# Optimization experiments

Hardware: AMD Instinct MI355X
Metric: run time of the kernel (lower is better)

Reference implementation:

```python
import jax, jax.numpy as jnp
import numpy as np

EMB_DIM = 1024
NUM_HEAD = 16
HEAD_DIM = EMB_DIM // NUM_HEAD
B, S = 2, 2048


def setup_inputs() -> dict:
    key = jax.random.key(0)
    ks = jax.random.split(key, 10)
    scale = 1.0 / np.sqrt(EMB_DIM)
    x = jax.random.normal(ks[0], (B, S, EMB_DIM), dtype=jnp.float32)
    # causal mask: 1 = keep, 0 = masked out (torch masked_fill(mask == 0, -inf))
    mask = jnp.tril(jnp.ones((S, S), dtype=jnp.int32))[None, None, :, :]
    def lin(kw, kb):
        W = jax.random.uniform(kw, (EMB_DIM, EMB_DIM), jnp.float32, -scale, scale)
        b = jax.random.uniform(kb, (EMB_DIM,), jnp.float32, -scale, scale)
        return W, b
    Wq, bq = lin(ks[1], ks[2])
    Wk, bk = lin(ks[3], ks[4])
    Wv, bv = lin(ks[5], ks[6])
    Wo, bo = lin(ks[7], ks[8])
    return {"x": x, "mask": mask, "Wq": Wq, "bq": bq, "Wk": Wk, "bk": bk,
            "Wv": Wv, "bv": bv, "Wo": Wo, "bo": bo}


def reference(x, mask, Wq, bq, Wk, bk, Wv, bv, Wo, bo):
    Bsz, Sq, _ = x.shape
    # projections; torch Linear: y = x @ W^T + b
    def proj(W, b):
        y = jnp.einsum('bse,fe->bsf', x, W) + b
        return y.reshape(Bsz, Sq, NUM_HEAD, HEAD_DIM).transpose(0, 2, 1, 3)  # [B,H,S,D]
    q = proj(Wq, bq)
    k = proj(Wk, bk)
    v = proj(Wv, bv)
    scaling = jnp.asarray(HEAD_DIM ** 0.5, x.dtype)
    scores = jnp.einsum('bhqd,bhkd->bhqk', q, k) / scaling  # [B,H,S,S]
    scores = jnp.where(mask == 0, -jnp.inf, scores)
    attn = jax.nn.softmax(scores, axis=-1)
    out = jnp.einsum('bhqk,bhkd->bhqd', attn, v)
    out = out.transpose(0, 2, 1, 3).reshape(Bsz, Sq, EMB_DIM)
    return jnp.einsum('bse,fe->bsf', out, Wo) + bo
```

## Files before the change

### kernel.cpp

```cpp
#include <hip/hip_runtime.h>

typedef unsigned short u16;
typedef __attribute__((ext_vector_type(8))) __bf16 bf16x8;
typedef __attribute__((ext_vector_type(8))) short  short8;
typedef __attribute__((ext_vector_type(4))) short  short4v;
typedef __attribute__((ext_vector_type(4))) float  floatx4;
typedef __attribute__((ext_vector_type(4))) int    intx4;

constexpr int Bc = 2, Sc = 2048, Ec = 1024, Hc = 16, Dc = 64;
constexpr int Mc = Bc * Sc;

#define QSCALE  0.18033688011112042f

__device__ __forceinline__ u16 f2b(float f) {
  union { float f; unsigned u; } c; c.f = f;
  unsigned u = c.u;
  return (u16)((u + 0x7fffu + ((u >> 16) & 1u)) >> 16);
}
__device__ __forceinline__ short8 ld8(const u16* p) { return *(const short8*)p; }

__device__ __forceinline__ int cvt_pk(float lo, float hi) {
  int r;
  asm("v_cvt_pk_bf16_f32 %0, %1, %2" : "=v"(r) : "v"(lo), "v"(hi));
  return r;
}

__device__ __forceinline__ floatx4 mfma16(short8 a, short8 b, floatx4 c) {
  return __builtin_amdgcn_mfma_f32_16x16x32_bf16(
      __builtin_bit_cast(bf16x8, a), __builtin_bit_cast(bf16x8, b), c, 0, 0, 0);
}

__device__ __forceinline__ void async16(const u16* g, u16* l) {
  __builtin_amdgcn_global_load_lds(
      (const __attribute__((address_space(1))) void*)g,
      (__attribute__((address_space(3))) void*)l, 16, 0, 0);
}

__global__ __launch_bounds__(256) void cvt_kernel(
    const float* __restrict__ x,  const float* __restrict__ Wq,
    const float* __restrict__ Wk, const float* __restrict__ Wv,
    const float* __restrict__ Wo, u16* __restrict__ dst) {
  const size_t i = ((size_t)blockIdx.x * 256 + threadIdx.x) * 4;
  const int seg = (int)(i >> 20);
  const float* src;
  size_t off;
  if (seg < 4)       { src = x;  off = i; }
  else if (seg == 4) { src = Wq; off = i - ((size_t)4 << 20); }
  else if (seg == 5) { src = Wk; off = i - ((size_t)5 << 20); }
  else if (seg == 6) { src = Wv; off = i - ((size_t)6 << 20); }
  else               { src = Wo; off = i - ((size_t)7 << 20); }
  floatx4 v = *(const floatx4*)(src + off);
  short4v o;
  o[0] = (short)f2b(v[0]); o[1] = (short)f2b(v[1]);
  o[2] = (short)f2b(v[2]); o[3] = (short)f2b(v[3]);
  *(short4v*)(dst + i) = o;
}

__device__ __forceinline__ void gemm128(
    const u16* __restrict__ A, const u16* __restrict__ B, int K,
    int m0, int n0, u16* As, u16* Bs, floatx4 acc[4][4]) {
  const int t = threadIdx.x;
  const int w = t >> 6, lane = t & 63;
  const int wm = w & 1, wn = w >> 1;
  const int quad = lane >> 4, l16 = lane & 15;
  const int r = t >> 2;
  const int c = ((t & 3) ^ ((t >> 3) & 3)) * 8;
  const int rsw = (l16 >> 1) & 3;

#pragma unroll
  for (int i = 0; i < 4; ++i)
#pragma unroll
    for (int j = 0; j < 4; ++j) acc[i][j] = 0.f;

#pragma unroll
  for (int jj = 0; jj < 2; ++jj) {
    async16(A + (size_t)(m0 + jj * 64 + r) * K + c, As + jj * 2048 + w * 512);
    async16(B + (size_t)(n0 + jj * 64 + r) * K + c, Bs + jj * 2048 + w * 512);
  }
  __syncthreads();

  int cur = 0;
  for (int k0 = 0; k0 < K; k0 += 32) {
    const int nxt = cur ^ 1;
    if (k0 + 32 < K) {
#pragma unroll
      for (int jj = 0; jj < 2; ++jj) {
        async16(A + (size_t)(m0 + jj * 64 + r) * K + (k0 + 32) + c,
                As + nxt * 4096 + jj * 2048 + w * 512);
        async16(B + (size_t)(n0 + jj * 64 + r) * K + (k0 + 32) + c,
                Bs + nxt * 4096 + jj * 2048 + w * 512);
      }
    }
    short8 af[4], bfr[4];
#pragma unroll
    for (int i = 0; i < 4; ++i)
      af[i]  = *(const short8*)(As + cur * 4096 +
                (wm * 64 + i * 16 + l16) * 32 + (quad ^ rsw) * 8);
#pragma unroll
    for (int j = 0; j < 4; ++j)
      bfr[j] = *(const short8*)(Bs + cur * 4096 +
                (wn * 64 + j * 16 + l16) * 32 + (quad ^ rsw) * 8);
#pragma unroll
    for (int i = 0; i < 4; ++i)
#pragma unroll
      for (int j = 0; j < 4; ++j)
        acc[i][j] = mfma16(af[i], bfr[j], acc[i][j]);
    __syncthreads();
    cur = nxt;
  }
}

__global__ __launch_bounds__(256) void qkv_mm(
    const u16* __restrict__ xb, const u16* __restrict__ Wb,
    const float* __restrict__ bq, const float* __restrict__ bk,
    const float* __restrict__ bv,
    u16* __restrict__ Q, u16* __restrict__ K_, u16* __restrict__ Vt) {
  __shared__ __align__(16) u16 As[8192], Bs[8192];
  const int z = blockIdx.z;
  const u16* W = Wb + ((size_t)z << 20);
  const float* bias = (z == 0) ? bq : (z == 1) ? bk : bv;
  const int m0 = blockIdx.y * 128, n0 = blockIdx.x * 128;

  floatx4 acc[4][4];
  gemm128(xb, W, Ec, m0, n0, As, Bs, acc);

  const int t = threadIdx.x, w = t >> 6, lane = t & 63;
  const int wm = w & 1, wn = w >> 1, quad = lane >> 4, l16 = lane & 15;

  if (z < 2) {
#pragma unroll
    for (int i = 0; i < 4; ++i)
#pragma unroll
      for (int j = 0; j < 4; ++j)
#pragma unroll
        for (int rr = 0; rr < 4; ++rr) {
          const int row = m0 + wm * 64 + i * 16 + quad * 4 + rr;
          const int col = n0 + wn * 64 + j * 16 + l16;
          float v = acc[i][j][rr] + bias[col];
          if (z == 0) v *= QSCALE;
          const int bb = row >> 11, s = row & (Sc - 1);
          const int h = col >> 6, d = col & (Dc - 1), bh = bb * Hc + h;
          ((z == 0) ? Q : K_)[((size_t)bh * Sc + s) * Dc + d] = f2b(v);
        }
  } else {
    u16* Tb = wn ? Bs : As;
#pragma unroll
    for (int j = 0; j < 4; ++j) {
      const int col_local = j * 16 + l16;
      const float bcol = bias[n0 + wn * 64 + col_local];
#pragma unroll
      for (int i = 0; i < 4; ++i) {
        const int blk  = wm * 8 + (i & 2) * 2 + quad;
        const int blks = (blk & 8) | ((blk & 7) ^ (col_local & 7));
        short4v o;
        o[0] = (short)f2b(acc[i][j][0] + bcol);
        o[1] = (short)f2b(acc[i][j][1] + bcol);
        o[2] = (short)f2b(acc[i][j][2] + bcol);
        o[3] = (short)f2b(acc[i][j][3] + bcol);
        *(short4v*)(Tb + col_local * 128 + blks * 8 + (i & 1) * 4) = o;
      }
    }
    __syncthreads();
    const int bb = m0 >> 11;
    const int s0 = m0 & (Sc - 1);
#pragma unroll
    for (int bi = 0; bi < 2; ++bi) {
      const u16* Tr = bi ? Bs : As;
#pragma unroll
      for (int cc = 0; cc < 4; ++cc) {
        const int cid = cc * 256 + t;
        const int dl = cid >> 4, sc = cid & 15;
        const int scs = (sc & 8) | ((sc & 7) ^ (dl & 7));
        const int col = n0 + bi * 64 + dl;
        const int h = col >> 6, d = col & (Dc - 1), bh = bb * Hc + h;
        *(short8*)(Vt + ((size_t)bh * Dc + d) * Sc + s0 + sc * 8) =
            *(const short8*)(Tr + dl * 128 + scs * 8);
      }
    }
  }
}

__global__ __launch_bounds__(256) void proj_mm(
    const u16* __restrict__ O, const u16* __restrict__ Wob,
    const float* __restrict__ bias, float* __restrict__ out) {
  __shared__ __align__(16) u16 As[8192], Bs[8192];
  const int m0 = blockIdx.y * 128, n0 = blockIdx.x * 128;

  floatx4 acc[4][4];
  gemm128(O, Wob, Ec, m0, n0, As, Bs, acc);

  const int t = threadIdx.x, w = t >> 6, lane = t & 63;
  const int wm = w & 1, wn = w >> 1, quad = lane >> 4, l16 = lane & 15;
#pragma unroll
  for (int i = 0; i < 4; ++i)
#pragma unroll
    for (int j = 0; j < 4; ++j)
#pragma unroll
      for (int rr = 0; rr < 4; ++rr) {
        const int row = m0 + wm * 64 + i * 16 + quad * 4 + rr;
        const int col = n0 + wn * 64 + j * 16 + l16;
        out[(size_t)row * Ec + col] = acc[i][j][rr] + bias[col];
      }
}

__global__ __launch_bounds__(256, 4) void attn_kernel(
    const u16* __restrict__ Q, const u16* __restrict__ K,
    const u16* __restrict__ Vt, u16* __restrict__ O) {
  const int v  = blockIdx.x & 31, g8 = blockIdx.x >> 5, kk = blockIdx.y;
  const int q1 = (kk & 2) ? ((v + 8) & 31) : v;
  const int qt = (kk & 1) ? (31 - q1) : q1;
  const int q0 = qt * 64;
  const int bh = kk * 8 + g8;
  const int bb = bh >> 4, h = bh & 15;

  const u16* Qh = Q  + (size_t)bh * Sc * Dc;
  const u16* Kh = K  + (size_t)bh * Sc * Dc;
  const u16* Vh = Vt + (size_t)bh * Dc * Sc;

  const int t = threadIdx.x;
  const int w = t >> 6, lane = t & 63;
  const int quad = lane >> 4, l16 = lane & 15;

  __shared__ __align__(16) u16 Ks[8192];
  __shared__ __align__(16) u16 Vs[8192];

  const int sr = w * 8 + (lane >> 3);
  const int sb = (lane & 7) ^ (lane >> 3);
  const int swz = l16 & 7;

  const u16* qrow_p = Qh + (size_t)(q0 + w * 16 + l16) * Dc;
  const short8 aq0 = ld8(qrow_p + quad * 8);
  const short8 aq1 = ld8(qrow_p + 32 + quad * 8);

  float   lrow = 0.f;
  floatx4 oacc[4];
#pragma unroll
  for (int dt = 0; dt < 4; ++dt) oacc[dt] = 0.f;

  for (int kt = 0; kt <= q0; kt += 128) {
#pragma unroll
    for (int st = 0; st < 2; ++st)
#pragma unroll
      for (int it = 0; it < 2; ++it) {
        const int r = it * 32 + sr;
        async16(Kh + (size_t)(kt + st * 64 + r) * Dc + sb * 8,
                Ks + st * 4096 + it * 2048 + w * 512);
        async16(Vh + (size_t)r * Sc + kt + st * 64 + sb * 8,
                Vs + st * 4096 + it * 2048 + w * 512);
      }
    __syncthreads();

    floatx4 sacc[8];
#pragma unroll
    for (int g = 0; g < 8; ++g) sacc[g] = 0.f;
#pragma unroll
    for (int ks = 0; ks < 2; ++ks) {
      const short8 bq = ks ? aq1 : aq0;
#pragma unroll
      for (int g = 0; g < 8; ++g) {
        const short8 a = *(const short8*)(
            Ks + (g >> 2) * 4096 + ((g & 3) * 16 + l16) * 64 +
            (((ks * 4 + quad) ^ swz) * 8));
        sacc[g] = mfma16(a, bq, sacc[g]);
      }
    }

    const bool diag = (kt + 128 > q0);
    const int thr = q0 + w * 16 + l16 - kt - 4 * quad;
#pragma unroll
    for (int g = 0; g < 8; ++g)
#pragma unroll
      for (int r = 0; r < 4; ++r) {
        float pv = exp2f(sacc[g][r]);
        if (diag && (16 * g + r > thr)) pv = 0.f;
        lrow += pv;
        sacc[g][r] = pv;
      }

    short8 pa[4];
#pragma unroll
    for (int c = 0; c < 4; ++c) {
      intx4 wd;
      wd[0] = cvt_pk(sacc[2 * c][0],     sacc[2 * c][1]);
      wd[1] = cvt_pk(sacc[2 * c][2],     sacc[2 * c][3]);
      wd[2] = cvt_pk(sacc[2 * c + 1][0], sacc[2 * c + 1][1]);
      wd[3] = cvt_pk(sacc[2 * c + 1][2], sacc[2 * c + 1][3]);
      pa[c] = __builtin_bit_cast(short8, wd);
    }

#pragma unroll
    for (int c = 0; c < 4; ++c) {
      const int st = c >> 1, kcl = c & 1;
#pragma unroll
      for (int dt = 0; dt < 4; ++dt) {
        const short8 b = *(const short8*)(
            Vs + st * 4096 + (dt * 16 + l16) * 64 +
            (((kcl * 4 + quad) ^ swz) * 8));
        oacc[dt] = mfma16(pa[c], b, oacc[dt]);
      }
    }
    __syncthreads();
  }

  lrow += __shfl_xor(lrow, 16);
  lrow += __shfl_xor(lrow, 32);
  float rs[4];
#pragma unroll
  for (int r = 0; r < 4; ++r)
    rs[r] = 1.f / __shfl(lrow, quad * 4 + r, 16);

#pragma unroll
  for (int dt = 0; dt < 4; ++dt) {
#pragma unroll
    for (int r = 0; r < 4; ++r) {
      const int qrow = q0 + w * 16 + quad * 4 + r;
      O[((size_t)(bb * Sc + qrow)) * Ec + h * Dc + dt * 16 + l16] =
          f2b(oacc[dt][r] * rs[r]);
    }
  }
}

extern "C" void kernel_launch(void* const* d_in, const int* in_sizes, int n_in,
                              void* d_out, int out_size, void* d_ws, size_t ws_size,
                              hipStream_t stream) {
  const float* x  = (const float*)d_in[0];
  const float* Wq = (const float*)d_in[2];
  const float* bq = (const float*)d_in[3];
  const float* Wk = (const float*)d_in[4];
  const float* bk = (const float*)d_in[5];
  const float* Wv = (const float*)d_in[6];
  const float* bv = (const float*)d_in[7];
  const float* Wo = (const float*)d_in[8];
  const float* bo = (const float*)d_in[9];

  const size_t MiE = (size_t)Mc * Ec;
  u16* Q  = (u16*)d_ws;
  u16* K  = Q  + MiE;
  u16* Vt = K  + MiE;
  u16* O  = Vt + MiE;
  u16* xb = O  + MiE;
  u16* Wb = xb + MiE;
  u16* Wob = Wb + ((size_t)3 << 20);

  cvt_kernel<<<8192, 256, 0, stream>>>(x, Wq, Wk, Wv, Wo, xb);
  qkv_mm<<<dim3(Ec / 128, Mc / 128, 3), 256, 0, stream>>>(
      xb, Wb, bq, bk, bv, Q, K, Vt);
  attn_kernel<<<dim3(256, 4), 256, 0, stream>>>(Q, K, Vt, O);
  proj_mm<<<dim3(Ec / 128, Mc / 128), 256, 0, stream>>>(O, Wob, bo, (float*)d_out);
}
```

Baseline: 214.3 us.

## Single-buffer GEMM LDS and remap blocks across XCDs for L2 locality

Removes double buffering in the shared GEMM loop, halving LDS per block from 32KB to 16KB so more blocks can reside per CU. The V-transpose epilogue is reworked to run in two passes through one 16KB buffer. Block indices are remapped so each XCD gets a contiguous range of M tiles, with the aim of improving L2 reuse of A rows. The cost is that global loads are no longer overlapped with MFMA compute within a block, so the loop now relies on occupancy for latency hiding.

```diff
diff --git a/kernel.cpp b/kernel.cpp
--- a/kernel.cpp
+++ b/kernel.cpp
@@ -72,42 +72,36 @@
 #pragma unroll
     for (int j = 0; j < 4; ++j) acc[i][j] = 0.f;
 
-#pragma unroll
-  for (int jj = 0; jj < 2; ++jj) {
-    async16(A + (size_t)(m0 + jj * 64 + r) * K + c, As + jj * 2048 + w * 512);
-    async16(B + (size_t)(n0 + jj * 64 + r) * K + c, Bs + jj * 2048 + w * 512);
-  }
-  __syncthreads();
-
-  int cur = 0;
   for (int k0 = 0; k0 < K; k0 += 32) {
-    const int nxt = cur ^ 1;
-    if (k0 + 32 < K) {
-#pragma unroll
-      for (int jj = 0; jj < 2; ++jj) {
-        async16(A + (size_t)(m0 + jj * 64 + r) * K + (k0 + 32) + c,
-                As + nxt * 4096 + jj * 2048 + w * 512);
-        async16(B + (size_t)(n0 + jj * 64 + r) * K + (k0 + 32) + c,
-                Bs + nxt * 4096 + jj * 2048 + w * 512);
-      }
-    }
+#pragma unroll
+    for (int jj = 0; jj < 2; ++jj) {
+      async16(A + (size_t)(m0 + jj * 64 + r) * K + k0 + c, As + jj * 2048 + w * 512);
+      async16(B + (size_t)(n0 + jj * 64 + r) * K + k0 + c, Bs + jj * 2048 + w * 512);
+    }
+    __syncthreads();
     short8 af[4], bfr[4];
 #pragma unroll
     for (int i = 0; i < 4; ++i)
-      af[i]  = *(const short8*)(As + cur * 4096 +
-                (wm * 64 + i * 16 + l16) * 32 + (quad ^ rsw) * 8);
+      af[i]  = *(const short8*)(As + (wm * 64 + i * 16 + l16) * 32 +
+                                (quad ^ rsw) * 8);
 #pragma unroll
     for (int j = 0; j < 4; ++j)
-      bfr[j] = *(const short8*)(Bs + cur * 4096 +
-                (wn * 64 + j * 16 + l16) * 32 + (quad ^ rsw) * 8);
+      bfr[j] = *(const short8*)(Bs + (wn * 64 + j * 16 + l16) * 32 +
+                                (quad ^ rsw) * 8);
 #pragma unroll
     for (int i = 0; i < 4; ++i)
 #pragma unroll
       for (int j = 0; j < 4; ++j)
         acc[i][j] = mfma16(af[i], bfr[j], acc[i][j]);
     __syncthreads();
-    cur = nxt;
   }
+}
+
+__device__ __forceinline__ void xcd_remap(int& m0, int& n0) {
+  const int id = blockIdx.x + (blockIdx.y << 3);
+  const int xcd = id & 7, slot = id >> 3;
+  n0 = (slot >> 2) * 128;
+  m0 = (xcd * 4 + (slot & 3)) * 128;
 }
 
 __global__ __launch_bounds__(256) void qkv_mm(
@@ -115,11 +109,14 @@
     const float* __restrict__ bq, const float* __restrict__ bk,
     const float* __restrict__ bv,
     u16* __restrict__ Q, u16* __restrict__ K_, u16* __restrict__ Vt) {
-  __shared__ __align__(16) u16 As[8192], Bs[8192];
+  __shared__ __align__(16) u16 S[8192];
+  u16* const As = S;
+  u16* const Bs = S + 4096;
   const int z = blockIdx.z;
   const u16* W = Wb + ((size_t)z << 20);
   const float* bias = (z == 0) ? bq : (z == 1) ? bk : bv;
-  const int m0 = blockIdx.y * 128, n0 = blockIdx.x * 128;
+  int m0, n0;
+  xcd_remap(m0, n0);
 
   floatx4 acc[4][4];
   gemm128(xb, W, Ec, m0, n0, As, Bs, acc);
@@ -143,38 +140,39 @@
           ((z == 0) ? Q : K_)[((size_t)bh * Sc + s) * Dc + d] = f2b(v);
         }
   } else {
-    u16* Tb = wn ? Bs : As;
-#pragma unroll
-    for (int j = 0; j < 4; ++j) {
-      const int col_local = j * 16 + l16;
-      const float bcol = bias[n0 + wn * 64 + col_local];
-#pragma unroll
-      for (int i = 0; i < 4; ++i) {
-        const int blk  = wm * 8 + (i & 2) * 2 + quad;
-        const int blks = (blk & 8) | ((blk & 7) ^ (col_local & 7));
-        short4v o;
-        o[0] = (short)f2b(acc[i][j][0] + bcol);
-        o[1] = (short)f2b(acc[i][j][1] + bcol);
-        o[2] = (short)f2b(acc[i][j][2] + bcol);
-        o[3] = (short)f2b(acc[i][j][3] + bcol);
-        *(short4v*)(Tb + col_local * 128 + blks * 8 + (i & 1) * 4) = o;
-      }
-    }
-    __syncthreads();
     const int bb = m0 >> 11;
     const int s0 = m0 & (Sc - 1);
 #pragma unroll
-    for (int bi = 0; bi < 2; ++bi) {
-      const u16* Tr = bi ? Bs : As;
+    for (int pass = 0; pass < 2; ++pass) {
+      __syncthreads();
+      if (wn == pass) {
+#pragma unroll
+        for (int j = 0; j < 4; ++j) {
+          const int col_local = j * 16 + l16;
+          const float bcol = bias[n0 + pass * 64 + col_local];
+#pragma unroll
+          for (int i = 0; i < 4; ++i) {
+            const int blk  = wm * 8 + (i & 2) * 2 + quad;
+            const int blks = (blk & 8) | ((blk & 7) ^ (col_local & 7));
+            short4v o;
+            o[0] = (short)f2b(acc[i][j][0] + bcol);
+            o[1] = (short)f2b(acc[i][j][1] + bcol);
+            o[2] = (short)f2b(acc[i][j][2] + bcol);
+            o[3] = (short)f2b(acc[i][j][3] + bcol);
+            *(short4v*)(S + col_local * 128 + blks * 8 + (i & 1) * 4) = o;
+          }
+        }
+      }
+      __syncthreads();
 #pragma unroll
       for (int cc = 0; cc < 4; ++cc) {
         const int cid = cc * 256 + t;
         const int dl = cid >> 4, sc = cid & 15;
         const int scs = (sc & 8) | ((sc & 7) ^ (dl & 7));
-        const int col = n0 + bi * 64 + dl;
+        const int col = n0 + pass * 64 + dl;
         const int h = col >> 6, d = col & (Dc - 1), bh = bb * Hc + h;
         *(short8*)(Vt + ((size_t)bh * Dc + d) * Sc + s0 + sc * 8) =
-            *(const short8*)(Tr + dl * 128 + scs * 8);
+            *(const short8*)(S + dl * 128 + scs * 8);
       }
     }
   }
@@ -183,8 +181,11 @@
 __global__ __launch_bounds__(256) void proj_mm(
     const u16* __restrict__ O, const u16* __restrict__ Wob,
     const float* __restrict__ bias, float* __restrict__ out) {
-  __shared__ __align__(16) u16 As[8192], Bs[8192];
-  const int m0 = blockIdx.y * 128, n0 = blockIdx.x * 128;
+  __shared__ __align__(16) u16 S[8192];
+  u16* const As = S;
+  u16* const Bs = S + 4096;
+  int m0, n0;
+  xcd_remap(m0, n0);
 
   floatx4 acc[4][4];
   gemm128(O, Wob, Ec, m0, n0, As, Bs, acc);
```

After: 222.4 us. +3.8%, slower.
